# Kernel optimization log

Hardware: AMD Instinct MI355X
Metric: run time of the kernel (lower is better)

Reference implementation:

```python
import jax, jax.numpy as jnp
import numpy as np

N = 50000
E = 800000
NODE_F = 128
HID = 96
TEMP_F = 10


def setup_inputs() -> dict:
    key = jax.random.key(0)
    ks = jax.random.split(key, 10)
    x = jax.random.normal(ks[0], (N, NODE_F), dtype=jnp.float32)
    edge_index = jax.random.randint(ks[1], (2, E), 0, N, dtype=jnp.int64)
    temporal = jax.random.normal(ks[2], (N, TEMP_F), dtype=jnp.float32)
    # GCNConv: lin weight [in, out] (no bias in lin), separate bias [out]
    W_gcn = jax.random.normal(ks[3], (NODE_F, HID), dtype=jnp.float32) / np.sqrt(NODE_F)
    b_gcn = jnp.zeros((HID,), dtype=jnp.float32)
    W1 = jax.random.normal(ks[4], (HID + TEMP_F, HID), dtype=jnp.float32) / np.sqrt(HID + TEMP_F)
    b1 = jax.random.normal(ks[5], (HID,), dtype=jnp.float32) * 0.01
    W2 = jax.random.normal(ks[6], (HID + NODE_F, 1), dtype=jnp.float32) / np.sqrt(HID + NODE_F)
    b2 = jax.random.normal(ks[7], (1,), dtype=jnp.float32) * 0.01
    return {"x": x, "edge_index": edge_index, "temporal": temporal,
            "W_gcn": W_gcn, "b_gcn": b_gcn, "W1": W1, "b1": b1, "W2": W2, "b2": b2}


def _gcn_conv(x, edge_index, W, b):
    n = x.shape[0]
    loop = jnp.arange(n, dtype=edge_index.dtype)
    src = jnp.concatenate([edge_index[0], loop])  # [E+N]
    dst = jnp.concatenate([edge_index[1], loop])
    # symmetric normalization with self-loops (PyG gcn_norm)
    ones = jnp.ones(src.shape[0], dtype=x.dtype)
    deg = jax.ops.segment_sum(ones, dst, num_segments=n)
    dinv = jnp.where(deg > 0, jax.lax.rsqrt(deg), 0.0)
    norm = dinv[src] * dinv[dst]  # [E+N]
    h = x @ W  # [N, HID]
    msg = h[src] * norm[:, None]  # [E+N, HID] gather + scale
    out = jax.ops.segment_sum(msg, dst, num_segments=n)  # scatter-add
    return out + b


def reference(x, edge_index, temporal, W_gcn, b_gcn, W1, b1, W2, b2):
    h = jax.nn.relu(_gcn_conv(x, edge_index, W_gcn, b_gcn))  # [N, HID]
    h = jnp.concatenate([h, temporal], axis=-1)              # [N, HID+TEMP_F]
    h = jax.nn.relu(h @ W1 + b1)                             # [N, HID]
    h = jnp.concatenate([h, x], axis=-1)                     # [N, HID+NODE_F]
    return jax.nn.relu(h @ W2 + b2)                          # [N, 1]
```

## Files before the change

kernel.cpp:

```cpp
#include <hip/hip_runtime.h>
#include <hip/hip_bf16.h>

#define NN 50000
#define NPAD 50048
#define NE 800000
#define NF 128
#define HH 96
#define TF 10
#define Z1DIM (HH + TF)
#define ZK 128
#define NCH 4
#define CW 24
#define NBK 196
#define CAP 5120
#define EPB 8192

typedef __attribute__((ext_vector_type(8))) short short8;
typedef __attribute__((ext_vector_type(8))) unsigned short ushort8;
typedef __attribute__((ext_vector_type(4))) float f32x4;

__device__ __forceinline__ float bu2f(unsigned short u) {
    union { unsigned int i; float f; } c;
    c.i = ((unsigned int)u) << 16;
    return c.f;
}
__device__ __forceinline__ unsigned short f2bu(float f) {
    union { __hip_bfloat16 h; unsigned short u; } c;
    c.h = __float2bfloat16(f);
    return c.u;
}

__global__ void k_init(int* __restrict__ bcur, int* __restrict__ off) {
    int t = threadIdx.x;
    if (t < NBK) bcur[t] = t * CAP;
    if (t == 255) off[NN] = NE;
}

__global__ __launch_bounds__(256) void k_fillA(const int* __restrict__ ei,
                                               int* __restrict__ bcur,
                                               int* __restrict__ temp) {
    __shared__ int hist[NBK], base[NBK];
    const int t = threadIdx.x;
    for (int m = t; m < NBK; m += 256) hist[m] = 0;
    __syncthreads();
    const int e0 = blockIdx.x * EPB;
    const int ecap = min(e0 + EPB, NE);
    for (int e = e0 + t; e < ecap; e += 256) {
        int d = ei[NE + e];
        atomicAdd(&hist[d >> 8], 1);
    }
    __syncthreads();
    for (int m = t; m < NBK; m += 256) {
        int c = hist[m];
        base[m] = c ? atomicAdd(&bcur[m], c) : 0;
        hist[m] = 0;
    }
    __syncthreads();
    for (int e = e0 + t; e < ecap; e += 256) {
        int d = ei[NE + e], s = ei[e];
        int b = d >> 8;
        int r = atomicAdd(&hist[b], 1);
        temp[base[b] + r] = ((d & 255) << 16) | s;
    }
}

__global__ __launch_bounds__(256) void k_gscan(const int* __restrict__ bcur,
                                               int* __restrict__ gbase) {
    __shared__ int p[256];
    const int t = threadIdx.x;
    int sz = (t < NBK) ? (bcur[t] - t * CAP) : 0;
    p[t] = sz;
    __syncthreads();
#pragma unroll
    for (int d = 1; d < 256; d <<= 1) {
        int u = (t >= d) ? p[t - d] : 0;
        __syncthreads();
        p[t] += u;
        __syncthreads();
    }
    if (t < NBK) gbase[t] = p[t] - sz;
}

__global__ __launch_bounds__(256) void k_fillB(const int* __restrict__ temp,
                                               const int* __restrict__ bcur,
                                               const int* __restrict__ gbase,
                                               unsigned short* __restrict__ csr,
                                               int* __restrict__ off) {
    __shared__ int ls[256], lc[256];
    const int b = blockIdx.x, t = threadIdx.x;
    const int seg0 = b * CAP;
    const int m = bcur[b] - seg0;
    const int g0 = gbase[b];
    ls[t] = 0;
    __syncthreads();
    for (int k = t; k < m; k += 256) atomicAdd(&ls[temp[seg0 + k] >> 16], 1);
    __syncthreads();
    const int myc = ls[t];
    lc[t] = myc;
    __syncthreads();
#pragma unroll
    for (int d = 1; d < 256; d <<= 1) {
        int u = (t >= d) ? lc[t - d] : 0;
        __syncthreads();
        lc[t] += u;
        __syncthreads();
    }
    const int myoff = lc[t] - myc;
    __syncthreads();
    lc[t] = myoff;
    const int i = b * 256 + t;
    if (i < NN) off[i] = g0 + myoff;
    __syncthreads();
    for (int k = t; k < m; k += 256) {
        int v = temp[seg0 + k];
        int r = atomicAdd(&lc[v >> 16], 1);
        csr[g0 + r] = (unsigned short)(v & 0xFFFF);
    }
}

#define WBLK (NF * HH / 4 / 256)
#define W1BLK (HH * ZK / 4 / 256)
#define ZTBLK (NPAD / 32)
#define ZPBLK 5
__global__ void k_prep(const float* __restrict__ W,
                       const float* __restrict__ W1, const float* __restrict__ tmp,
                       unsigned short* __restrict__ Wt,
                       unsigned short* __restrict__ Wt1, unsigned short* __restrict__ zb) {
    int b = blockIdx.x;
    if (b < WBLK) {
        int e = (b * 256 + threadIdx.x) * 4;
        int n = e >> 7, k = e & 127;
        ushort4 v;
        v.x = f2bu(W[(k + 0) * HH + n]);
        v.y = f2bu(W[(k + 1) * HH + n]);
        v.z = f2bu(W[(k + 2) * HH + n]);
        v.w = f2bu(W[(k + 3) * HH + n]);
        *(ushort4*)(Wt + e) = v;
    } else if (b < WBLK + W1BLK) {
        int e = ((b - WBLK) * 256 + threadIdx.x) * 4;
        int n = e >> 7, k = e & 127;
        ushort4 v;
        v.x = (k + 0 < Z1DIM) ? f2bu(W1[(k + 0) * HH + n]) : (unsigned short)0;
        v.y = (k + 1 < Z1DIM) ? f2bu(W1[(k + 1) * HH + n]) : (unsigned short)0;
        v.z = (k + 2 < Z1DIM) ? f2bu(W1[(k + 2) * HH + n]) : (unsigned short)0;
        v.w = (k + 3 < Z1DIM) ? f2bu(W1[(k + 3) * HH + n]) : (unsigned short)0;
        *(ushort4*)(Wt1 + e) = v;
    } else if (b < WBLK + W1BLK + ZTBLK) {
        int t4 = ((b - WBLK - W1BLK) * 256 + threadIdx.x) * 4;
        int i = t4 >> 5, cc = t4 & 31;
        ushort4 v; v.x = v.y = v.z = v.w = 0;
        if (i < NN) {
            if (cc + 0 < TF) v.x = f2bu(tmp[(size_t)i * TF + cc + 0]);
            if (cc + 1 < TF) v.y = f2bu(tmp[(size_t)i * TF + cc + 1]);
            if (cc + 2 < TF) v.z = f2bu(tmp[(size_t)i * TF + cc + 2]);
            if (cc + 3 < TF) v.w = f2bu(tmp[(size_t)i * TF + cc + 3]);
        }
        *(ushort4*)(zb + (size_t)i * ZK + HH + cc) = v;
    } else {
        int t4 = ((b - WBLK - W1BLK - ZTBLK) * 256 + threadIdx.x) * 4;
        if (t4 < (NPAD - NN) * HH) {
            int i = NN + t4 / HH, j = t4 % HH;
            ushort4 z; z.x = z.y = z.z = z.w = 0;
            *(ushort4*)(zb + (size_t)i * ZK + j) = z;
        }
    }
}

__global__ __launch_bounds__(256) void k_gemm(const float* __restrict__ x,
                                              const unsigned short* __restrict__ Wt,
                                              const int* __restrict__ off,
                                              const float* __restrict__ W2,
                                              unsigned short* __restrict__ hp_c,
                                              float* __restrict__ xw2) {
    const int wave = threadIdx.x >> 6;
    const int lane = threadIdx.x & 63;
    const int quad = lane >> 4;
    const int l16 = lane & 15;
    const int Mbase = blockIdx.x * 64 + wave * 16;
    const int row = Mbase + l16;
    const bool valid = row < NN;

    const float* xr = x + (size_t)row * NF + quad * 8;
    const unsigned short* brow = Wt + (size_t)l16 * NF + quad * 8;

    f32x4 acc[6] = {};
    float xs = 0.f;
#pragma unroll
    for (int ks = 0; ks < 4; ++ks) {
        short8 a = {};
        if (valid) {
            float4 f0 = *(const float4*)(xr + ks * 32);
            float4 f1 = *(const float4*)(xr + ks * 32 + 4);
            const float4 w0 = *(const float4*)(W2 + HH + quad * 8 + ks * 32);
            const float4 w1 = *(const float4*)(W2 + HH + quad * 8 + ks * 32 + 4);
            xs = fmaf(f0.x, w0.x, xs); xs = fmaf(f0.y, w0.y, xs);
            xs = fmaf(f0.z, w0.z, xs); xs = fmaf(f0.w, w0.w, xs);
            xs = fmaf(f1.x, w1.x, xs); xs = fmaf(f1.y, w1.y, xs);
            xs = fmaf(f1.z, w1.z, xs); xs = fmaf(f1.w, w1.w, xs);
            a[0] = (short)f2bu(f0.x); a[1] = (short)f2bu(f0.y);
            a[2] = (short)f2bu(f0.z); a[3] = (short)f2bu(f0.w);
            a[4] = (short)f2bu(f1.x); a[5] = (short)f2bu(f1.y);
            a[6] = (short)f2bu(f1.z); a[7] = (short)f2bu(f1.w);
        }
#pragma unroll
        for (int nt = 0; nt < 6; ++nt) {
            short8 bfrag = *(const short8*)(brow + (size_t)nt * 16 * NF + ks * 32);
            acc[nt] = __builtin_amdgcn_mfma_f32_16x16x32_bf16(a, bfrag, acc[nt], 0, 0, 0);
        }
    }
    xs += __shfl_xor(xs, 16, 64);
    xs += __shfl_xor(xs, 32, 64);
    if (quad == 0 && valid) xw2[row] = xs;

    const int r0 = Mbase + quad * 4;
    float dv[4];
#pragma unroll
    for (int k = 0; k < 4; ++k) {
        int r = r0 + k;
        dv[k] = (r < NN) ? rsqrtf((float)(off[r + 1] - off[r]) + 1.f) : 0.f;
    }
#pragma unroll
    for (int nt = 0; nt < 6; ++nt) {
        int n = nt * 16 + l16;
        int c = n / CW, jj = n - c * CW;
        unsigned short* dst = hp_c + (size_t)c * NN * CW + jj;
#pragma unroll
        for (int k = 0; k < 4; ++k)
            if (r0 + k < NN) dst[(size_t)(r0 + k) * CW] = f2bu(acc[nt][k] * dv[k]);
    }
}

#define RPC 586
#define AGGB (4 * RPC)
__global__ __launch_bounds__(256) void k_agg(const unsigned short* __restrict__ hp_c,
                                             const int* __restrict__ off,
                                             const unsigned short* __restrict__ csr,
                                             const float* __restrict__ bg,
                                             unsigned short* __restrict__ zb) {
    const int b = blockIdx.x;
    const int slot = b & 7;
    const int c = slot >> 1;
    const int r = (b >> 3) * 2 + (slot & 1);
    const int item = r * 256 + threadIdx.x;
    if (item >= NN * 3) return;
    const int i = item / 3;
    const int q = item - i * 3;
    const unsigned short* base = hp_c + (size_t)c * NN * CW + q * 8;

    ushort8 sv = *(const ushort8*)(base + (size_t)i * CW);
    float a0 = bu2f(sv[0]), a1 = bu2f(sv[1]), a2 = bu2f(sv[2]), a3 = bu2f(sv[3]);
    float a4 = bu2f(sv[4]), a5 = bu2f(sv[5]), a6 = bu2f(sv[6]), a7 = bu2f(sv[7]);

    int idx = off[i];
    const int end = off[i + 1];
    const float dv = rsqrtf((float)(end - idx) + 1.f);
    for (; idx + 3 < end; idx += 4) {
        int s0 = csr[idx], s1 = csr[idx + 1], s2 = csr[idx + 2], s3 = csr[idx + 3];
        ushort8 v0 = *(const ushort8*)(base + (size_t)s0 * CW);
        ushort8 v1 = *(const ushort8*)(base + (size_t)s1 * CW);
        ushort8 v2 = *(const ushort8*)(base + (size_t)s2 * CW);
        ushort8 v3 = *(const ushort8*)(base + (size_t)s3 * CW);
        a0 += (bu2f(v0[0]) + bu2f(v1[0])) + (bu2f(v2[0]) + bu2f(v3[0]));
        a1 += (bu2f(v0[1]) + bu2f(v1[1])) + (bu2f(v2[1]) + bu2f(v3[1]));
        a2 += (bu2f(v0[2]) + bu2f(v1[2])) + (bu2f(v2[2]) + bu2f(v3[2]));
        a3 += (bu2f(v0[3]) + bu2f(v1[3])) + (bu2f(v2[3]) + bu2f(v3[3]));
        a4 += (bu2f(v0[4]) + bu2f(v1[4])) + (bu2f(v2[4]) + bu2f(v3[4]));
        a5 += (bu2f(v0[5]) + bu2f(v1[5])) + (bu2f(v2[5]) + bu2f(v3[5]));
        a6 += (bu2f(v0[6]) + bu2f(v1[6])) + (bu2f(v2[6]) + bu2f(v3[6]));
        a7 += (bu2f(v0[7]) + bu2f(v1[7])) + (bu2f(v2[7]) + bu2f(v3[7]));
    }
    for (; idx < end; ++idx) {
        ushort8 v0 = *(const ushort8*)(base + (size_t)csr[idx] * CW);
        a0 += bu2f(v0[0]); a1 += bu2f(v0[1]); a2 += bu2f(v0[2]); a3 += bu2f(v0[3]);
        a4 += bu2f(v0[4]); a5 += bu2f(v0[5]); a6 += bu2f(v0[6]); a7 += bu2f(v0[7]);
    }
    const int j = c * CW + q * 8;
    ushort8 o;
    o[0] = f2bu(fmaxf(fmaf(dv, a0, bg[j + 0]), 0.f));
    o[1] = f2bu(fmaxf(fmaf(dv, a1, bg[j + 1]), 0.f));
    o[2] = f2bu(fmaxf(fmaf(dv, a2, bg[j + 2]), 0.f));
    o[3] = f2bu(fmaxf(fmaf(dv, a3, bg[j + 3]), 0.f));
    o[4] = f2bu(fmaxf(fmaf(dv, a4, bg[j + 4]), 0.f));
    o[5] = f2bu(fmaxf(fmaf(dv, a5, bg[j + 5]), 0.f));
    o[6] = f2bu(fmaxf(fmaf(dv, a6, bg[j + 6]), 0.f));
    o[7] = f2bu(fmaxf(fmaf(dv, a7, bg[j + 7]), 0.f));
    *(ushort8*)(zb + (size_t)i * ZK + j) = o;
}

__global__ __launch_bounds__(256) void k_mlp2(const unsigned short* __restrict__ zb,
                                              const unsigned short* __restrict__ Wt1,
                                              const float* __restrict__ b1,
                                              const float* __restrict__ W2,
                                              const float* __restrict__ b2,
                                              const float* __restrict__ xw2,
                                              float* __restrict__ out) {
    const int wave = threadIdx.x >> 6;
    const int lane = threadIdx.x & 63;
    const int quad = lane >> 4;
    const int l16 = lane & 15;
    const int Mbase = blockIdx.x * 64 + wave * 16;

    const unsigned short* arow = zb + (size_t)(Mbase + l16) * ZK + quad * 8;
    const unsigned short* brow = Wt1 + (size_t)l16 * ZK + quad * 8;

    f32x4 acc[6] = {};
#pragma unroll
    for (int ks = 0; ks < 4; ++ks) {
        short8 a = *(const short8*)(arow + ks * 32);
#pragma unroll
        for (int nt = 0; nt < 6; ++nt) {
            short8 bfrag = *(const short8*)(brow + (size_t)nt * 16 * ZK + ks * 32);
            acc[nt] = __builtin_amdgcn_mfma_f32_16x16x32_bf16(a, bfrag, acc[nt], 0, 0, 0);
        }
    }
    float bb[6], wa[6];
#pragma unroll
    for (int nt = 0; nt < 6; ++nt) {
        int c = nt * 16 + l16;
        bb[nt] = b1[c];
        wa[nt] = W2[c];
    }
    const float bias2 = b2[0];

#pragma unroll
    for (int reg = 0; reg < 4; ++reg) {
        const int r = Mbase + quad * 4 + reg;
        float p = 0.f;
#pragma unroll
        for (int nt = 0; nt < 6; ++nt)
            p = fmaf(fmaxf(acc[nt][reg] + bb[nt], 0.f), wa[nt], p);
#pragma unroll
        for (int m = 1; m < 16; m <<= 1) p += __shfl_xor(p, m, 64);
        if (l16 == 0 && r < NN) out[r] = fmaxf(p + xw2[r] + bias2, 0.f);
    }
}

extern "C" void kernel_launch(void* const* d_in, const int* in_sizes, int n_in,
                              void* d_out, int out_size, void* d_ws, size_t ws_size,
                              hipStream_t stream) {
    const float* x   = (const float*)d_in[0];
    const int*   ei  = (const int*)d_in[1];
    const float* tmp = (const float*)d_in[2];
    const float* Wg  = (const float*)d_in[3];
    const float* bg  = (const float*)d_in[4];
    const float* W1  = (const float*)d_in[5];
    const float* b1  = (const float*)d_in[6];
    const float* W2  = (const float*)d_in[7];
    const float* b2  = (const float*)d_in[8];
    float* out = (float*)d_out;

    char* base = (char*)d_ws;
    int* off  = (int*)base;
    int* bcur = off + 65536;
    int* gbase = bcur + 256;
    unsigned short* csr = (unsigned short*)(gbase + 256);
    unsigned short* Wt  = (unsigned short*)(base + ((size_t)4 << 20));
    unsigned short* Wt1 = Wt + NF * HH;
    unsigned short* hp_c = Wt1 + HH * ZK;
    unsigned short* zb = hp_c + (size_t)NN * HH;
    float* xw2 = (float*)(zb + (size_t)NPAD * ZK);
    int* temp = (int*)zb;

    k_init <<<1, 256, 0, stream>>>(bcur, off);
    k_fillA<<<(NE + EPB - 1) / EPB, 256, 0, stream>>>(ei, bcur, temp);
    k_gscan<<<1, 256, 0, stream>>>(bcur, gbase);
    k_fillB<<<NBK, 256, 0, stream>>>(temp, bcur, gbase, csr, off);
    k_prep <<<WBLK + W1BLK + ZTBLK + ZPBLK, 256, 0, stream>>>(Wg, W1, tmp, Wt, Wt1, zb);
    k_gemm <<<NPAD / 64, 256, 0, stream>>>(x, Wt, off, W2, hp_c, xw2);
    k_agg  <<<AGGB, 256, 0, stream>>>(hp_c, off, csr, bg, zb);
    k_mlp2 <<<NPAD / 64, 256, 0, stream>>>(zb, Wt1, b1, W2, b2, xw2, out);
}
```

Before: 185.9 us.

## Fold bucket scan into fillB and split each node's edge list across two lanes

Removes the single-block k_gscan launch by having every k_fillB block redundantly compute the bucket prefix scan in shared memory. In k_agg, each (node, 8-column chunk) item is now handled by two adjacent lanes that walk alternate CSR edges, and their partial sums are combined with a lane shuffle before the store. The aim is to cut one launch and to raise memory-level parallelism in the gather-bound aggregation. The cost is twice as many threads with shorter loops, redundant scan work in every fillB block, and half the lanes idle during the store.

```diff
diff --git a/kernel.cpp b/kernel.cpp
--- a/kernel.cpp
+++ b/kernel.cpp
@@ -64,35 +64,28 @@
     }
 }
 
-__global__ __launch_bounds__(256) void k_gscan(const int* __restrict__ bcur,
-                                               int* __restrict__ gbase) {
-    __shared__ int p[256];
-    const int t = threadIdx.x;
-    int sz = (t < NBK) ? (bcur[t] - t * CAP) : 0;
-    p[t] = sz;
-    __syncthreads();
-#pragma unroll
-    for (int d = 1; d < 256; d <<= 1) {
-        int u = (t >= d) ? p[t - d] : 0;
-        __syncthreads();
-        p[t] += u;
-        __syncthreads();
-    }
-    if (t < NBK) gbase[t] = p[t] - sz;
-}
-
 __global__ __launch_bounds__(256) void k_fillB(const int* __restrict__ temp,
                                                const int* __restrict__ bcur,
-                                               const int* __restrict__ gbase,
                                                unsigned short* __restrict__ csr,
                                                int* __restrict__ off) {
     __shared__ int ls[256], lc[256];
     const int b = blockIdx.x, t = threadIdx.x;
+    int szt = (t < NBK) ? (bcur[t] - t * CAP) : 0;
+    ls[t] = szt;
+    __syncthreads();
+#pragma unroll
+    for (int d = 1; d < 256; d <<= 1) {
+        int u = (t >= d) ? ls[t - d] : 0;
+        __syncthreads();
+        ls[t] += u;
+        __syncthreads();
+    }
+    const int g0 = (b > 0) ? ls[b - 1] : 0;
+    __syncthreads();
+    ls[t] = 0;
+    __syncthreads();
     const int seg0 = b * CAP;
     const int m = bcur[b] - seg0;
-    const int g0 = gbase[b];
-    ls[t] = 0;
-    __syncthreads();
     for (int k = t; k < m; k += 256) atomicAdd(&ls[temp[seg0 + k] >> 16], 1);
     __syncthreads();
     const int myc = ls[t];
@@ -230,8 +223,8 @@
     }
 }
 
-#define RPC 586
-#define AGGB (4 * RPC)
+#define RPC2 1172
+#define AGGB (4 * RPC2)
 __global__ __launch_bounds__(256) void k_agg(const unsigned short* __restrict__ hp_c,
                                              const int* __restrict__ off,
                                              const unsigned short* __restrict__ csr,
@@ -242,20 +235,28 @@
     const int c = slot >> 1;
     const int r = (b >> 3) * 2 + (slot & 1);
     const int item = r * 256 + threadIdx.x;
-    if (item >= NN * 3) return;
-    const int i = item / 3;
-    const int q = item - i * 3;
+    if (item >= NN * 6) return;
+    const int i = item / 6;
+    const int sub = item - i * 6;
+    const int q = sub >> 1;
+    const int h = sub & 1;
     const unsigned short* base = hp_c + (size_t)c * NN * CW + q * 8;
 
-    ushort8 sv = *(const ushort8*)(base + (size_t)i * CW);
-    float a0 = bu2f(sv[0]), a1 = bu2f(sv[1]), a2 = bu2f(sv[2]), a3 = bu2f(sv[3]);
-    float a4 = bu2f(sv[4]), a5 = bu2f(sv[5]), a6 = bu2f(sv[6]), a7 = bu2f(sv[7]);
-
-    int idx = off[i];
+    float a0, a1, a2, a3, a4, a5, a6, a7;
+    if (h == 0) {
+        ushort8 sv = *(const ushort8*)(base + (size_t)i * CW);
+        a0 = bu2f(sv[0]); a1 = bu2f(sv[1]); a2 = bu2f(sv[2]); a3 = bu2f(sv[3]);
+        a4 = bu2f(sv[4]); a5 = bu2f(sv[5]); a6 = bu2f(sv[6]); a7 = bu2f(sv[7]);
+    } else {
+        a0 = a1 = a2 = a3 = a4 = a5 = a6 = a7 = 0.f;
+    }
+
+    const int start = off[i];
     const int end = off[i + 1];
-    const float dv = rsqrtf((float)(end - idx) + 1.f);
-    for (; idx + 3 < end; idx += 4) {
-        int s0 = csr[idx], s1 = csr[idx + 1], s2 = csr[idx + 2], s3 = csr[idx + 3];
+    const float dv = rsqrtf((float)(end - start) + 1.f);
+    int k = start + h;
+    for (; k + 6 < end; k += 8) {
+        int s0 = csr[k], s1 = csr[k + 2], s2 = csr[k + 4], s3 = csr[k + 6];
         ushort8 v0 = *(const ushort8*)(base + (size_t)s0 * CW);
         ushort8 v1 = *(const ushort8*)(base + (size_t)s1 * CW);
         ushort8 v2 = *(const ushort8*)(base + (size_t)s2 * CW);
@@ -269,22 +270,28 @@
         a6 += (bu2f(v0[6]) + bu2f(v1[6])) + (bu2f(v2[6]) + bu2f(v3[6]));
         a7 += (bu2f(v0[7]) + bu2f(v1[7])) + (bu2f(v2[7]) + bu2f(v3[7]));
     }
-    for (; idx < end; ++idx) {
-        ushort8 v0 = *(const ushort8*)(base + (size_t)csr[idx] * CW);
+    for (; k < end; k += 2) {
+        ushort8 v0 = *(const ushort8*)(base + (size_t)csr[k] * CW);
         a0 += bu2f(v0[0]); a1 += bu2f(v0[1]); a2 += bu2f(v0[2]); a3 += bu2f(v0[3]);
         a4 += bu2f(v0[4]); a5 += bu2f(v0[5]); a6 += bu2f(v0[6]); a7 += bu2f(v0[7]);
     }
-    const int j = c * CW + q * 8;
-    ushort8 o;
-    o[0] = f2bu(fmaxf(fmaf(dv, a0, bg[j + 0]), 0.f));
-    o[1] = f2bu(fmaxf(fmaf(dv, a1, bg[j + 1]), 0.f));
-    o[2] = f2bu(fmaxf(fmaf(dv, a2, bg[j + 2]), 0.f));
-    o[3] = f2bu(fmaxf(fmaf(dv, a3, bg[j + 3]), 0.f));
-    o[4] = f2bu(fmaxf(fmaf(dv, a4, bg[j + 4]), 0.f));
-    o[5] = f2bu(fmaxf(fmaf(dv, a5, bg[j + 5]), 0.f));
-    o[6] = f2bu(fmaxf(fmaf(dv, a6, bg[j + 6]), 0.f));
-    o[7] = f2bu(fmaxf(fmaf(dv, a7, bg[j + 7]), 0.f));
-    *(ushort8*)(zb + (size_t)i * ZK + j) = o;
+    a0 += __shfl_xor(a0, 1, 64); a1 += __shfl_xor(a1, 1, 64);
+    a2 += __shfl_xor(a2, 1, 64); a3 += __shfl_xor(a3, 1, 64);
+    a4 += __shfl_xor(a4, 1, 64); a5 += __shfl_xor(a5, 1, 64);
+    a6 += __shfl_xor(a6, 1, 64); a7 += __shfl_xor(a7, 1, 64);
+    if (h == 0) {
+        const int j = c * CW + q * 8;
+        ushort8 o;
+        o[0] = f2bu(fmaxf(fmaf(dv, a0, bg[j + 0]), 0.f));
+        o[1] = f2bu(fmaxf(fmaf(dv, a1, bg[j + 1]), 0.f));
+        o[2] = f2bu(fmaxf(fmaf(dv, a2, bg[j + 2]), 0.f));
+        o[3] = f2bu(fmaxf(fmaf(dv, a3, bg[j + 3]), 0.f));
+        o[4] = f2bu(fmaxf(fmaf(dv, a4, bg[j + 4]), 0.f));
+        o[5] = f2bu(fmaxf(fmaf(dv, a5, bg[j + 5]), 0.f));
+        o[6] = f2bu(fmaxf(fmaf(dv, a6, bg[j + 6]), 0.f));
+        o[7] = f2bu(fmaxf(fmaf(dv, a7, bg[j + 7]), 0.f));
+        *(ushort8*)(zb + (size_t)i * ZK + j) = o;
+    }
 }
 
 __global__ __launch_bounds__(256) void k_mlp2(const unsigned short* __restrict__ zb,
@@ -352,8 +359,7 @@
     char* base = (char*)d_ws;
     int* off  = (int*)base;
     int* bcur = off + 65536;
-    int* gbase = bcur + 256;
-    unsigned short* csr = (unsigned short*)(gbase + 256);
+    unsigned short* csr = (unsigned short*)(bcur + 512);
     unsigned short* Wt  = (unsigned short*)(base + ((size_t)4 << 20));
     unsigned short* Wt1 = Wt + NF * HH;
     unsigned short* hp_c = Wt1 + HH * ZK;
@@ -363,8 +369,7 @@
 
     k_init <<<1, 256, 0, stream>>>(bcur, off);
     k_fillA<<<(NE + EPB - 1) / EPB, 256, 0, stream>>>(ei, bcur, temp);
-    k_gscan<<<1, 256, 0, stream>>>(bcur, gbase);
-    k_fillB<<<NBK, 256, 0, stream>>>(temp, bcur, gbase, csr, off);
+    k_fillB<<<NBK, 256, 0, stream>>>(temp, bcur, csr, off);
     k_prep <<<WBLK + W1BLK + ZTBLK + ZPBLK, 256, 0, stream>>>(Wg, W1, tmp, Wt, Wt1, zb);
     k_gemm <<<NPAD / 64, 256, 0, stream>>>(x, Wt, off, W2, hp_c, xw2);
     k_agg  <<<AGGB, 256, 0, stream>>>(hp_c, off, csr, bg, zb);
```

After: 182.3 us. Within noise of the previous version (-1.9%).
